# Kernel optimization log

Hardware: AMD Instinct MI355X
Metric: run time of the kernel (lower is better)

Reference implementation:

```python
import jax, jax.numpy as jnp
import numpy as np

DEPTH = 6
N_LEAF = 2 ** DEPTH          # 64
GATE_COUNT = N_LEAF - 1      # 63
IN_F = 512
OUT_F = 512
BATCH = 1024


def setup_inputs() -> dict:
    key = jax.random.key(0)
    k1, k2, k3 = jax.random.split(key, 3)
    x = jax.random.normal(k1, (BATCH, IN_F), dtype=jnp.float32)
    gw = jax.random.normal(k2, (IN_F, GATE_COUNT), dtype=jnp.float32)
    gb = jnp.zeros((GATE_COUNT,), dtype=jnp.float32)
    pw = jax.random.normal(k3, (OUT_F, IN_F, N_LEAF), dtype=jnp.float32)
    pb = jnp.zeros((OUT_F, N_LEAF), dtype=jnp.float32)
    return {"x": x, "gw": gw, "gb": gb, "pw": pw, "pb": pb}


def _leaf_probs(x, gw, gb, depth):
    # gatings: sigmoid(x @ gw + gb), shape [B, gate_count]
    g = jax.nn.sigmoid(x @ gw + gb)
    B = x.shape[0]
    dens = jnp.ones((B, 1), dtype=x.dtype)  # root density
    offset = 0
    for d in range(depth):
        n = 2 ** d
        gp = g[:, offset:offset + n]                    # parent gatings [B, n]
        # left child multiplies by g, right child by (1 - g), interleaved
        pair = jnp.stack([gp, 1.0 - gp], axis=-1).reshape(B, 2 * n)
        dens = jnp.repeat(dens, 2, axis=1) * pair        # [B, 2n]
        offset += n
    return dens  # [B, n_leaf]


def reference(x, gw, gb, pw, pb):
    leaf = _leaf_probs(x, gw, gb, DEPTH)                 # [B, L]
    # per-leaf linear projections, then mix with leaf probabilities
    y = jnp.einsum('bi,oil->bol', x, pw)                 # [B, O, L]
    out = jnp.einsum('bol,bl->bo', y, leaf) + leaf @ pb.T
    return out
```

## Files before the change

### kernel.cpp

```cpp
#include <hip/hip_runtime.h>
#include <hip/hip_bf16.h>

#define TDEPTH 6
#define NLEAF 64
#define NGATE 63
#define INF 512
#define OUTF 512
#define BATCH 1024

#define BM 256
#define BN 128
#define SPLITK 16
#define KCH 513
#define THREADS 512
#define XPITCH 36
#define BPITCH 144

typedef __attribute__((ext_vector_type(4))) float f32x4;
typedef __attribute__((ext_vector_type(8))) __bf16 bf16x8;

__global__ __launch_bounds__(256) void leaf_kernel(
    const float* __restrict__ x, const float* __restrict__ gw,
    const float* __restrict__ gb, float* __restrict__ leaf) {
  const int wid = threadIdx.x >> 6, lane = threadIdx.x & 63;
  const int b = blockIdx.x * 4 + wid;
  __shared__ float g[4][NLEAF];
  if (lane < NGATE) {
    const float* xr = x + (size_t)b * INF;
    float a0 = 0.f, a1 = 0.f, a2 = 0.f, a3 = 0.f;
    #pragma unroll 4
    for (int i = 0; i < INF; i += 4) {
      a0 += xr[i + 0] * gw[(i + 0) * NGATE + lane];
      a1 += xr[i + 1] * gw[(i + 1) * NGATE + lane];
      a2 += xr[i + 2] * gw[(i + 2) * NGATE + lane];
      a3 += xr[i + 3] * gw[(i + 3) * NGATE + lane];
    }
    float t = (a0 + a1) + (a2 + a3) + gb[lane];
    g[wid][lane] = 1.0f / (1.0f + __expf(-t));
  }
  __syncthreads();
  float p = 1.0f;
  #pragma unroll
  for (int d = 0; d < TDEPTH; d++) {
    int prefix = lane >> (TDEPTH - 1 - d);
    int node = (1 << d) - 1 + (prefix >> 1);
    float gv = g[wid][node];
    p *= (prefix & 1) ? (1.0f - gv) : gv;
  }
  leaf[(size_t)b * NLEAF + lane] = p;
}

__device__ __forceinline__ void sync_raw() {
  asm volatile("s_waitcnt lgkmcnt(0)" ::: "memory");
  __builtin_amdgcn_sched_barrier(0);
  __builtin_amdgcn_s_barrier();
  __builtin_amdgcn_sched_barrier(0);
}

__global__ __launch_bounds__(THREADS, 2) void gemm_kernel(
    const float* __restrict__ x, const float* __restrict__ pw,
    const float* __restrict__ pb, const float* __restrict__ leaf,
    float* __restrict__ partial) {
  __shared__ __align__(16) float xsm[BM * XPITCH];
  __shared__ __align__(16) __bf16 Bsm[2][BN * (BPITCH / 2)];

  const int tid = threadIdx.x;
  const int lane = tid & 63;
  const int wid = tid >> 6;
  const int wm = wid >> 1, wn = wid & 1;
  const int q = lane >> 4, rl = lane & 15;

  const int bid = blockIdx.x;
  const int L = (bid & 7) * 32 + (bid >> 3);
  const int mb = L & 3, g = L >> 2;
  const int nb = g >> 4, s = g & 15;
  const int m0 = mb * BM, n0 = nb * BN;
  const int cs = (s * KCH) / SPLITK;
  const int ce = ((s + 1) * KCH) / SPLITK;
  const int nreal = min(ce, INF) - cs;
  const int total = nreal + ((ce == KCH) ? 1 : 0);

  f32x4 lf[4][2][2];
  #pragma unroll
  for (int mi = 0; mi < 4; mi++) {
    const float* lr = leaf + (size_t)(m0 + wm * 64 + mi * 16 + rl) * NLEAF + q * 8;
    #pragma unroll
    for (int kk = 0; kk < 2; kk++) {
      lf[mi][kk][0] = *(const f32x4*)(lr + kk * 32);
      lf[mi][kk][1] = *(const f32x4*)(lr + kk * 32 + 4);
    }
  }

  const int bo = tid >> 2, bc = tid & 3;
  const float* pwrow = pw + (size_t)(n0 + bo) * (INF * NLEAF) + bc * 16;
  const float* pbrow = pb + (size_t)(n0 + bo) * NLEAF + bc * 16;

  f32x4 acc[4][4];
  #pragma unroll
  for (int mi = 0; mi < 4; mi++)
    #pragma unroll
    for (int ni = 0; ni < 4; ni++) acc[mi][ni] = (f32x4){0.f, 0.f, 0.f, 0.f};

  f32x4 bvA[4], bvB[4];

  {
    const float* s0 = pwrow + (size_t)cs * NLEAF;
    #pragma unroll
    for (int j = 0; j < 4; j++) bvA[j] = *(const f32x4*)(s0 + j * 4);
    const float* s1 = pwrow + (size_t)(cs + 1) * NLEAF;
    #pragma unroll
    for (int j = 0; j < 4; j++) bvB[j] = *(const f32x4*)(s1 + j * 4);
  }
  {
    int r = tid >> 1, h = tid & 1;
    const float* src = x + (size_t)(m0 + r) * INF + cs + h * 16;
    float* dst = xsm + r * XPITCH + h * 16;
    #pragma unroll
    for (int j = 0; j < 4; j++)
      *(f32x4*)(dst + j * 4) = *(const f32x4*)(src + j * 4);
  }
  {
    #pragma unroll
    for (int h = 0; h < 2; h++) {
      f32x4 lo = bvA[2 * h], hi = bvA[2 * h + 1];
      bf16x8 w;
      w[0] = (__bf16)lo[0]; w[1] = (__bf16)lo[1];
      w[2] = (__bf16)lo[2]; w[3] = (__bf16)lo[3];
      w[4] = (__bf16)hi[0]; w[5] = (__bf16)hi[1];
      w[6] = (__bf16)hi[2]; w[7] = (__bf16)hi[3];
      *(bf16x8*)((char*)&Bsm[0][0] + bo * BPITCH + bc * 32 + h * 16) = w;
    }
  }
  sync_raw();

  auto step_body = [&](int t, f32x4(&Rld)[4], f32x4(&Rst)[4],
                       __bf16* cur, __bf16* nxt) {
    if (t + 2 < total) {
      const float* s2 = (t + 2 < nreal)
          ? pwrow + (size_t)(cs + t + 2) * NLEAF : pbrow;
      #pragma unroll
      for (int j = 0; j < 4; j++) Rld[j] = *(const f32x4*)(s2 + j * 4);
    }
    float xv[4];
    #pragma unroll
    for (int mi = 0; mi < 4; mi++) {
      float v = xsm[(wm * 64 + mi * 16 + rl) * XPITCH + (t & 31)];
      xv[mi] = (t < nreal) ? v : 1.0f;
    }
    #pragma unroll
    for (int kk = 0; kk < 2; kk++) {
      bf16x8 bfr[4];
      #pragma unroll
      for (int ni = 0; ni < 4; ni++) {
        int row = wn * 64 + ni * 16 + rl;
        bfr[ni] = *(const bf16x8*)((const char*)cur + row * BPITCH +
                                   kk * 64 + q * 16);
      }
      #pragma unroll
      for (int mi = 0; mi < 4; mi++) {
        f32x4 p0 = lf[mi][kk][0] * xv[mi];
        f32x4 p1 = lf[mi][kk][1] * xv[mi];
        bf16x8 a;
        a[0] = (__bf16)p0[0]; a[1] = (__bf16)p0[1];
        a[2] = (__bf16)p0[2]; a[3] = (__bf16)p0[3];
        a[4] = (__bf16)p1[0]; a[5] = (__bf16)p1[1];
        a[6] = (__bf16)p1[2]; a[7] = (__bf16)p1[3];
        #pragma unroll
        for (int ni = 0; ni < 4; ni++)
          acc[mi][ni] = __builtin_amdgcn_mfma_f32_16x16x32_bf16(
              a, bfr[ni], acc[mi][ni], 0, 0, 0);
      }
    }
    if (t + 1 < total) {
      #pragma unroll
      for (int h = 0; h < 2; h++) {
        f32x4 lo = Rst[2 * h], hi = Rst[2 * h + 1];
        bf16x8 w;
        w[0] = (__bf16)lo[0]; w[1] = (__bf16)lo[1];
        w[2] = (__bf16)lo[2]; w[3] = (__bf16)lo[3];
        w[4] = (__bf16)hi[0]; w[5] = (__bf16)hi[1];
        w[6] = (__bf16)hi[2]; w[7] = (__bf16)hi[3];
        *(bf16x8*)((char*)nxt + bo * BPITCH + bc * 32 + h * 16) = w;
      }
    }
    sync_raw();
  };

  __bf16* B0 = &Bsm[0][0];
  __bf16* B1 = &Bsm[1][0];
  for (int t = 0; t < total; t += 2) {
    step_body(t, bvA, bvB, B0, B1);
    if (t + 1 < total) step_body(t + 1, bvB, bvA, B1, B0);
  }

  float* dst = partial + ((size_t)s * BATCH + m0) * OUTF + n0;
  #pragma unroll
  for (int mi = 0; mi < 4; mi++)
    #pragma unroll
    for (int ni = 0; ni < 4; ni++)
      #pragma unroll
      for (int r = 0; r < 4; r++) {
        int row = wm * 64 + mi * 16 + q * 4 + r;
        int col = wn * 64 + ni * 16 + rl;
        dst[(size_t)row * OUTF + col] = acc[mi][ni][r];
      }
}

__global__ __launch_bounds__(256) void reduce_kernel(
    const float* __restrict__ partial, float* __restrict__ out) {
  size_t e = ((size_t)blockIdx.x * 256 + threadIdx.x) * 4;
  f32x4 sum = (f32x4){0.f, 0.f, 0.f, 0.f};
  #pragma unroll
  for (int s = 0; s < SPLITK; s++)
    sum += *(const f32x4*)(partial + (size_t)s * BATCH * OUTF + e);
  *(f32x4*)(out + e) = sum;
}

extern "C" void kernel_launch(void* const* d_in, const int* in_sizes, int n_in,
                              void* d_out, int out_size, void* d_ws, size_t ws_size,
                              hipStream_t stream) {
  const float* x  = (const float*)d_in[0];
  const float* gw = (const float*)d_in[1];
  const float* gb = (const float*)d_in[2];
  const float* pw = (const float*)d_in[3];
  const float* pb = (const float*)d_in[4];
  float* out = (float*)d_out;

  float* leaf    = (float*)d_ws;
  float* partial = (float*)((char*)d_ws + (1 << 19));

  leaf_kernel<<<BATCH / 4, 256, 0, stream>>>(x, gw, gb, leaf);
  gemm_kernel<<<(BATCH / BM) * (OUTF / BN) * SPLITK, THREADS, 0, stream>>>(
      x, pw, pb, leaf, partial);
  reduce_kernel<<<(BATCH * OUTF) / (256 * 4), 256, 0, stream>>>(partial, out);
}
```

Measured before the change: 72.34 us.

## Use 32x32x16 bf16 MFMA with smaller 128x64 tiles and more blocks

Reshapes the split-K GEMM tile from 256x128 with 512 threads to 128x64 with 256 threads. Each wave now computes a 32x64 output strip using 32x32x16 bf16 MFMAs instead of a grid of 16x16x32 ones. The pw prefetch drops from two steps ahead to one, and the two-step unrolled lambda becomes a simple loop. The goal is 1024 blocks with higher occupancy for better latency hiding. The cost is less reuse of each staged B tile across rows, so pw is re-read from global memory more times, and the shorter prefetch distance gives less time to hide load latency.

New measurement: 74.38 us. +2.8%, slower.

```diff
diff --git a/kernel.cpp b/kernel.cpp
--- a/kernel.cpp
+++ b/kernel.cpp
@@ -8,16 +8,17 @@
 #define OUTF 512
 #define BATCH 1024
 
-#define BM 256
-#define BN 128
+#define BM 128
+#define BN 64
 #define SPLITK 16
 #define KCH 513
-#define THREADS 512
+#define THREADS 256
 #define XPITCH 36
 #define BPITCH 144
 
-typedef __attribute__((ext_vector_type(4))) float f32x4;
-typedef __attribute__((ext_vector_type(8))) __bf16 bf16x8;
+typedef __attribute__((ext_vector_type(4)))  float f32x4;
+typedef __attribute__((ext_vector_type(16))) float f32x16;
+typedef __attribute__((ext_vector_type(8)))  __bf16 bf16x8;
 
 __global__ __launch_bounds__(256) void leaf_kernel(
     const float* __restrict__ x, const float* __restrict__ gw,
@@ -57,60 +58,39 @@
   __builtin_amdgcn_sched_barrier(0);
 }
 
-__global__ __launch_bounds__(THREADS, 2) void gemm_kernel(
+__global__ __launch_bounds__(THREADS, 4) void gemm_kernel(
     const float* __restrict__ x, const float* __restrict__ pw,
     const float* __restrict__ pb, const float* __restrict__ leaf,
     float* __restrict__ partial) {
   __shared__ __align__(16) float xsm[BM * XPITCH];
-  __shared__ __align__(16) __bf16 Bsm[2][BN * (BPITCH / 2)];
+  __shared__ __align__(16) __bf16 Bsm[2][BN * (BPITCH/2)];
 
   const int tid = threadIdx.x;
   const int lane = tid & 63;
   const int wid = tid >> 6;
-  const int wm = wid >> 1, wn = wid & 1;
-  const int q = lane >> 4, rl = lane & 15;
+  const int lo = lane & 31;
+  const int half = lane >> 5;
 
   const int bid = blockIdx.x;
-  const int L = (bid & 7) * 32 + (bid >> 3);
-  const int mb = L & 3, g = L >> 2;
-  const int nb = g >> 4, s = g & 15;
+  const int nb = bid & 7, mb = (bid >> 3) & 7, s = bid >> 6;
   const int m0 = mb * BM, n0 = nb * BN;
   const int cs = (s * KCH) / SPLITK;
   const int ce = ((s + 1) * KCH) / SPLITK;
   const int nreal = min(ce, INF) - cs;
   const int total = nreal + ((ce == KCH) ? 1 : 0);
 
-  f32x4 lf[4][2][2];
-  #pragma unroll
-  for (int mi = 0; mi < 4; mi++) {
-    const float* lr = leaf + (size_t)(m0 + wm * 64 + mi * 16 + rl) * NLEAF + q * 8;
-    #pragma unroll
-    for (int kk = 0; kk < 2; kk++) {
-      lf[mi][kk][0] = *(const f32x4*)(lr + kk * 32);
-      lf[mi][kk][1] = *(const f32x4*)(lr + kk * 32 + 4);
-    }
-  }
-
-  const int bo = tid >> 2, bc = tid & 3;
-  const float* pwrow = pw + (size_t)(n0 + bo) * (INF * NLEAF) + bc * 16;
-  const float* pbrow = pb + (size_t)(n0 + bo) * NLEAF + bc * 16;
-
-  f32x4 acc[4][4];
-  #pragma unroll
-  for (int mi = 0; mi < 4; mi++)
-    #pragma unroll
-    for (int ni = 0; ni < 4; ni++) acc[mi][ni] = (f32x4){0.f, 0.f, 0.f, 0.f};
-
-  f32x4 bvA[4], bvB[4];
-
+  const int xrow = wid * 32 + lo;
+
+  f32x4 lf[4][2];
   {
-    const float* s0 = pwrow + (size_t)cs * NLEAF;
-    #pragma unroll
-    for (int j = 0; j < 4; j++) bvA[j] = *(const f32x4*)(s0 + j * 4);
-    const float* s1 = pwrow + (size_t)(cs + 1) * NLEAF;
-    #pragma unroll
-    for (int j = 0; j < 4; j++) bvB[j] = *(const f32x4*)(s1 + j * 4);
-  }
+    const float* lr = leaf + (size_t)(m0 + xrow) * NLEAF + half * 8;
+    #pragma unroll
+    for (int t4 = 0; t4 < 4; t4++) {
+      lf[t4][0] = *(const f32x4*)(lr + t4 * 16);
+      lf[t4][1] = *(const f32x4*)(lr + t4 * 16 + 4);
+    }
+  }
+
   {
     int r = tid >> 1, h = tid & 1;
     const float* src = x + (size_t)(m0 + r) * INF + cs + h * 16;
@@ -119,91 +99,86 @@
     for (int j = 0; j < 4; j++)
       *(f32x4*)(dst + j * 4) = *(const f32x4*)(src + j * 4);
   }
+
+  const int bo = tid >> 2, bc = tid & 3;
+  const float* pwrow = pw + (size_t)(n0 + bo) * (INF * NLEAF) + bc * 16;
+  const float* pbrow = pb + (size_t)(n0 + bo) * NLEAF + bc * 16;
+
+  f32x16 acc0 = (f32x16)(0.f), acc1 = (f32x16)(0.f);
+
+  f32x4 bv[4];
   {
+    const float* sp = pwrow + (size_t)cs * NLEAF;
+    #pragma unroll
+    for (int j = 0; j < 4; j++) bv[j] = *(const f32x4*)(sp + j * 4);
     #pragma unroll
     for (int h = 0; h < 2; h++) {
-      f32x4 lo = bvA[2 * h], hi = bvA[2 * h + 1];
+      f32x4 a = bv[2 * h], b = bv[2 * h + 1];
       bf16x8 w;
-      w[0] = (__bf16)lo[0]; w[1] = (__bf16)lo[1];
-      w[2] = (__bf16)lo[2]; w[3] = (__bf16)lo[3];
-      w[4] = (__bf16)hi[0]; w[5] = (__bf16)hi[1];
-      w[6] = (__bf16)hi[2]; w[7] = (__bf16)hi[3];
+      w[0] = (__bf16)a[0]; w[1] = (__bf16)a[1];
+      w[2] = (__bf16)a[2]; w[3] = (__bf16)a[3];
+      w[4] = (__bf16)b[0]; w[5] = (__bf16)b[1];
+      w[6] = (__bf16)b[2]; w[7] = (__bf16)b[3];
       *(bf16x8*)((char*)&Bsm[0][0] + bo * BPITCH + bc * 32 + h * 16) = w;
     }
   }
   sync_raw();
 
-  auto step_body = [&](int t, f32x4(&Rld)[4], f32x4(&Rst)[4],
-                       __bf16* cur, __bf16* nxt) {
-    if (t + 2 < total) {
-      const float* s2 = (t + 2 < nreal)
-          ? pwrow + (size_t)(cs + t + 2) * NLEAF : pbrow;
+  __bf16* cur = &Bsm[0][0];
+  __bf16* nxt = &Bsm[1][0];
+  for (int t = 0; t < total; ++t) {
+    const bool more = (t + 1 < total);
+    if (more) {
+      const float* sp = (t + 1 < nreal)
+          ? pwrow + (size_t)(cs + t + 1) * NLEAF : pbrow;
       #pragma unroll
-      for (int j = 0; j < 4; j++) Rld[j] = *(const f32x4*)(s2 + j * 4);
-    }
-    float xv[4];
-    #pragma unroll
-    for (int mi = 0; mi < 4; mi++) {
-      float v = xsm[(wm * 64 + mi * 16 + rl) * XPITCH + (t & 31)];
-      xv[mi] = (t < nreal) ? v : 1.0f;
-    }
-    #pragma unroll
-    for (int kk = 0; kk < 2; kk++) {
-      bf16x8 bfr[4];
-      #pragma unroll
-      for (int ni = 0; ni < 4; ni++) {
-        int row = wn * 64 + ni * 16 + rl;
-        bfr[ni] = *(const bf16x8*)((const char*)cur + row * BPITCH +
-                                   kk * 64 + q * 16);
-      }
-      #pragma unroll
-      for (int mi = 0; mi < 4; mi++) {
-        f32x4 p0 = lf[mi][kk][0] * xv[mi];
-        f32x4 p1 = lf[mi][kk][1] * xv[mi];
-        bf16x8 a;
-        a[0] = (__bf16)p0[0]; a[1] = (__bf16)p0[1];
-        a[2] = (__bf16)p0[2]; a[3] = (__bf16)p0[3];
-        a[4] = (__bf16)p1[0]; a[5] = (__bf16)p1[1];
-        a[6] = (__bf16)p1[2]; a[7] = (__bf16)p1[3];
-        #pragma unroll
-        for (int ni = 0; ni < 4; ni++)
-          acc[mi][ni] = __builtin_amdgcn_mfma_f32_16x16x32_bf16(
-              a, bfr[ni], acc[mi][ni], 0, 0, 0);
-      }
-    }
-    if (t + 1 < total) {
+      for (int j = 0; j < 4; j++) bv[j] = *(const f32x4*)(sp + j * 4);
+    }
+    float xvr = xsm[xrow * XPITCH + (t & 31)];
+    float xv = (t < nreal) ? xvr : 1.0f;
+    bf16x8 afr[4];
+    #pragma unroll
+    for (int t4 = 0; t4 < 4; t4++) {
+      f32x4 p0 = lf[t4][0] * xv, p1 = lf[t4][1] * xv;
+      bf16x8 a;
+      a[0] = (__bf16)p0[0]; a[1] = (__bf16)p0[1];
+      a[2] = (__bf16)p0[2]; a[3] = (__bf16)p0[3];
+      a[4] = (__bf16)p1[0]; a[5] = (__bf16)p1[1];
+      a[6] = (__bf16)p1[2]; a[7] = (__bf16)p1[3];
+      afr[t4] = a;
+    }
+    #pragma unroll
+    for (int t4 = 0; t4 < 4; t4++) {
+      bf16x8 b0 = *(const bf16x8*)((const char*)cur + lo * BPITCH +
+                                   t4 * 32 + half * 16);
+      bf16x8 b1 = *(const bf16x8*)((const char*)cur + (32 + lo) * BPITCH +
+                                   t4 * 32 + half * 16);
+      acc0 = __builtin_amdgcn_mfma_f32_32x32x16_bf16(afr[t4], b0, acc0, 0, 0, 0);
+      acc1 = __builtin_amdgcn_mfma_f32_32x32x16_bf16(afr[t4], b1, acc1, 0, 0, 0);
+    }
+    if (more) {
       #pragma unroll
       for (int h = 0; h < 2; h++) {
-        f32x4 lo = Rst[2 * h], hi = Rst[2 * h + 1];
+        f32x4 a = bv[2 * h], b = bv[2 * h + 1];
         bf16x8 w;
-        w[0] = (__bf16)lo[0]; w[1] = (__bf16)lo[1];
-        w[2] = (__bf16)lo[2]; w[3] = (__bf16)lo[3];
-        w[4] = (__bf16)hi[0]; w[5] = (__bf16)hi[1];
-        w[6] = (__bf16)hi[2]; w[7] = (__bf16)hi[3];
+        w[0] = (__bf16)a[0]; w[1] = (__bf16)a[1];
+        w[2] = (__bf16)a[2]; w[3] = (__bf16)a[3];
+        w[4] = (__bf16)b[0]; w[5] = (__bf16)b[1];
+        w[6] = (__bf16)b[2]; w[7] = (__bf16)b[3];
         *(bf16x8*)((char*)nxt + bo * BPITCH + bc * 32 + h * 16) = w;
       }
     }
     sync_raw();
-  };
-
-  __bf16* B0 = &Bsm[0][0];
-  __bf16* B1 = &Bsm[1][0];
-  for (int t = 0; t < total; t += 2) {
-    step_body(t, bvA, bvB, B0, B1);
-    if (t + 1 < total) step_body(t + 1, bvB, bvA, B1, B0);
-  }
-
-  float* dst = partial + ((size_t)s * BATCH + m0) * OUTF + n0;
+    __bf16* tmp = cur; cur = nxt; nxt = tmp;
+  }
+
+  float* dst = partial + ((size_t)s * BATCH + m0 + wid * 32) * OUTF + n0;
   #pragma unroll
-  for (int mi = 0; mi < 4; mi++)
-    #pragma unroll
-    for (int ni = 0; ni < 4; ni++)
-      #pragma unroll
-      for (int r = 0; r < 4; r++) {
-        int row = wm * 64 + mi * 16 + q * 4 + r;
-        int col = wn * 64 + ni * 16 + rl;
-        dst[(size_t)row * OUTF + col] = acc[mi][ni][r];
-      }
+  for (int e = 0; e < 16; e++) {
+    int row = (e & 3) + 8 * (e >> 2) + 4 * half;
+    dst[(size_t)row * OUTF + lo] = acc0[e];
+    dst[(size_t)row * OUTF + 32 + lo] = acc1[e];
+  }
 }
 
 __global__ __launch_bounds__(256) void reduce_kernel(
```
